# Kernel tuning notes

Hardware: AMD Instinct MI355X
Metric: run time of the kernel (lower is better)

Reference implementation:

```python
import jax, jax.numpy as jnp
import numpy as np

N_NODES = 50000
N_GRAPHS = 512


def _glorot(key, shape):
    fan_in, fan_out = shape[0], shape[1]
    lim = float(np.sqrt(6.0 / (fan_in + fan_out)))
    return jax.random.uniform(key, shape, jnp.float32, -lim, lim)


def setup_inputs() -> dict:
    key = jax.random.key(0)
    ks = jax.random.split(key, 12)
    x = jax.random.normal(ks[0], (N_NODES, 64), jnp.float32)
    edge_index = jax.random.randint(ks[1], (2, 800000), 0, N_NODES, jnp.int64)
    batch = jnp.sort(jax.random.randint(ks[2], (N_NODES,), 0, N_GRAPHS, jnp.int64))
    # GCNConv weights stored as [in, out]; bias [out]
    W1 = _glorot(ks[3], (64, 128));  b1 = jnp.zeros((128,), jnp.float32)
    W2 = _glorot(ks[4], (128, 128)); b2 = jnp.zeros((128,), jnp.float32)
    W3 = _glorot(ks[5], (128, 64));  b3 = jnp.zeros((64,), jnp.float32)
    Wl = _glorot(ks[6], (64, 10));   bl = jnp.zeros((10,), jnp.float32)
    return {"x": x, "edge_index": edge_index, "batch": batch,
            "W1": W1, "b1": b1, "W2": W2, "b2": b2,
            "W3": W3, "b3": b3, "Wl": Wl, "bl": bl}


def _gcn_conv(h_in, W, b, row, col, dinv, n):
    # GCNConv: out = D^{-1/2} (A + I) D^{-1/2} (X W) + b, self-loops folded in
    h = h_in @ W                                   # [N, out]
    norm = (dinv[row] * dinv[col])[:, None]        # [E, 1]
    agg = jax.ops.segment_sum(h[row] * norm, col, num_segments=n)
    agg = agg + (dinv * dinv)[:, None] * h          # self-loop contribution
    return agg + b


def reference(x, edge_index, batch, W1, b1, W2, b2, W3, b3, Wl, bl):
    n = x.shape[0]
    row, col = edge_index[0], edge_index[1]
    # degree of target nodes, including self loop
    deg = jax.ops.segment_sum(jnp.ones((row.shape[0],), x.dtype), col,
                              num_segments=n) + 1.0
    dinv = deg ** -0.5

    h = jax.nn.relu(_gcn_conv(x, W1, b1, row, col, dinv, n))
    h = jax.nn.relu(_gcn_conv(h, W2, b2, row, col, dinv, n))
    h = _gcn_conv(h, W3, b3, row, col, dinv, n)

    # global mean pool over graphs
    sums = jax.ops.segment_sum(h, batch, num_segments=N_GRAPHS)
    cnts = jax.ops.segment_sum(jnp.ones((n,), h.dtype), batch,
                               num_segments=N_GRAPHS)
    pooled = sums / jnp.maximum(cnts, 1.0)[:, None]
    # dropout is identity in eval mode
    return pooled @ Wl + bl
```

## Files before the change

### kernel.cpp

```cpp
#include <hip/hip_runtime.h>
#include <hip/hip_fp16.h>

typedef _Float16 f16;
typedef f16 f16x8 __attribute__((ext_vector_type(8)));
typedef float f32x4 __attribute__((ext_vector_type(4)));


__global__ void k_zero_i32(int* __restrict__ p, int n) {
    int i = blockIdx.x * blockDim.x + threadIdx.x;
    if (i < n) p[i] = 0;
}

__global__ void k_count(const int* __restrict__ col, int E, int* __restrict__ cnt) {
    int e = blockIdx.x * blockDim.x + threadIdx.x;
    if (e < E) atomicAdd(&cnt[col[e]], 1);
}

__global__ void k_bsum(const int* __restrict__ cnt, int N, int* __restrict__ bsum) {
    __shared__ int wt[4];
    int t = threadIdx.x;
    int i0 = blockIdx.x * 1024 + t * 4;
    int s = 0;
    #pragma unroll
    for (int j = 0; j < 4; ++j) { int i = i0 + j; if (i < N) s += cnt[i]; }
    #pragma unroll
    for (int off = 32; off > 0; off >>= 1) s += __shfl_down(s, off, 64);
    if ((t & 63) == 0) wt[t >> 6] = s;
    __syncthreads();
    if (t == 0) bsum[blockIdx.x] = wt[0] + wt[1] + wt[2] + wt[3];
}

__global__ void k_bscan(int* __restrict__ bsum, int nb, int* __restrict__ starts, int N) {
    int lane = threadIdx.x;
    int carry = 0;
    for (int base = 0; base < nb; base += 64) {
        int i = base + lane;
        int v = (i < nb) ? bsum[i] : 0;
        int s = v;
        #pragma unroll
        for (int off = 1; off < 64; off <<= 1) {
            int u = __shfl_up(s, off, 64);
            if (lane >= off) s += u;
        }
        if (i < nb) bsum[i] = carry + s - v;
        carry += __shfl(s, 63, 64);
    }
    if (lane == 0) starts[N] = carry;
}

__global__ void k_scan_apply(const int* __restrict__ cnt, const int* __restrict__ bsum,
                             int* __restrict__ starts, float* __restrict__ dinv, int N) {
    __shared__ int wt[4];
    int t = threadIdx.x;
    int lane = t & 63;
    int w = t >> 6;
    int i0 = blockIdx.x * 1024 + t * 4;
    int v[4];
    int ts = 0;
    #pragma unroll
    for (int j = 0; j < 4; ++j) { int i = i0 + j; v[j] = (i < N) ? cnt[i] : 0; ts += v[j]; }
    int s = ts;
    #pragma unroll
    for (int off = 1; off < 64; off <<= 1) {
        int u = __shfl_up(s, off, 64);
        if (lane >= off) s += u;
    }
    if (lane == 63) wt[w] = s;
    __syncthreads();
    int woff = 0;
    if (w > 0) woff = wt[0];
    if (w > 1) woff += wt[1];
    if (w > 2) woff += wt[2];
    int base = bsum[blockIdx.x] + woff + (s - ts);
    int run = base;
    #pragma unroll
    for (int j = 0; j < 4; ++j) {
        int i = i0 + j;
        if (i < N) {
            starts[i] = run;
            dinv[i] = rsqrtf((float)v[j] + 1.0f);
        }
        run += v[j];
    }
}

__global__ void k_fill_xcd(const int* __restrict__ row, const int* __restrict__ col, int E,
                           const int* __restrict__ starts, int* __restrict__ cnt,
                           int* __restrict__ csr, int N) {
    const int w = blockIdx.x & 7;
    const int chunk = blockIdx.x >> 3;
    const int nchunks = gridDim.x >> 3;
    const int W = (N + 7) / 8;
    const int c0 = w * W;
    const int c1 = min(N, c0 + W);
    const int stride = nchunks * blockDim.x;
    for (int e = chunk * blockDim.x + threadIdx.x; e < E; e += stride) {
        int c = col[e];
        if (c >= c0 && c < c1) {
            int pos = starts[c] + atomicSub(&cnt[c], 1) - 1;
            csr[pos] = row[e];
        }
    }
}

__global__ void k_prep(const float* __restrict__ x, __half* __restrict__ X16, long nx4,
                       const float* __restrict__ W1, const float* __restrict__ W2,
                       const float* __restrict__ W3, f16* __restrict__ Wt1,
                       f16* __restrict__ Wt2, f16* __restrict__ Wt3,
                       float* __restrict__ pooled, int npool) {
    long idx = (long)blockIdx.x * blockDim.x + threadIdx.x;
    if (idx < nx4) {
        long i = idx * 4;
        float4 v = *(const float4*)&x[i];
        __half2 h0 = __floats2half2_rn(v.x, v.y);
        __half2 h1 = __floats2half2_rn(v.z, v.w);
        uint2 q; q.x = *(unsigned int*)&h0; q.y = *(unsigned int*)&h1;
        *(uint2*)&X16[i] = q;
        return;
    }
    long j = idx - nx4;
    if (j < 32768) {
        if (j < 8192) {
            int k = (int)(j >> 7), m = (int)(j & 127);
            Wt1[m * 72 + k] = (f16)W1[j];
        } else if (j < 24576) {
            long u = j - 8192;
            int k = (int)(u >> 7), m = (int)(u & 127);
            Wt2[m * 136 + k] = (f16)W2[u];
        } else {
            long u = j - 24576;
            int k = (int)(u >> 6), m = (int)(u & 63);
            Wt3[m * 136 + k] = (f16)W3[u];
        }
        return;
    }
    long z = j - 32768;
    if (z < npool) pooled[z] = 0.0f;
}


template<int K, int M, bool BIAS, bool RELU, typename OT>
__global__ __launch_bounds__(256) void k_gemm_mfma(const f16* __restrict__ A,
                                                   const f16* __restrict__ Wt,
                                                   const float* __restrict__ bias,
                                                   OT* __restrict__ P, int N) {
    constexpr int KP = K + 8;
    constexpr int KK = K / 32;
    __shared__ f16 Wl[M * KP];
    const int t = threadIdx.x;
    constexpr int CH = (M * KP * 2) / 16;
    {
        const uint4* src = (const uint4*)Wt;
        uint4* dst = (uint4*)Wl;
        for (int i = t; i < CH; i += 256) dst[i] = src[i];
    }
    __syncthreads();
    const int lane = t & 63;
    const int wave = t >> 6;
    const int r = lane & 15;
    const int q = lane >> 4;
    const int arow = blockIdx.x * 64 + wave * 16 + r;
    f16x8 a[KK];
    #pragma unroll
    for (int kk = 0; kk < KK; ++kk) {
        if (arow < N) a[kk] = *(const f16x8*)&A[(long)arow * K + kk * 32 + q * 8];
        else { f16x8 z = {0, 0, 0, 0, 0, 0, 0, 0}; a[kk] = z; }
    }
    const int drow0 = blockIdx.x * 64 + wave * 16 + q * 4;
    #pragma unroll
    for (int ct = 0; ct < M / 16; ++ct) {
        const int col = ct * 16 + r;
        f32x4 acc = {0.f, 0.f, 0.f, 0.f};
        #pragma unroll
        for (int kk = 0; kk < KK; ++kk) {
            f16x8 b = *(const f16x8*)&Wl[col * KP + kk * 32 + q * 8];
            acc = __builtin_amdgcn_mfma_f32_16x16x32_f16(a[kk], b, acc, 0, 0, 0);
        }
        float bb = BIAS ? bias[col] : 0.f;
        #pragma unroll
        for (int g = 0; g < 4; ++g) {
            int rr = drow0 + g;
            if (rr < N) {
                float v = acc[g] + bb;
                if (RELU) v = fmaxf(v, 0.f);
                if constexpr (__is_same(OT, f16)) P[(long)rr * M + col] = (f16)v;
                else P[(long)rr * M + col] = v;
            }
        }
    }
}


template<int M, bool BIAS, bool RELU, typename OT>
__global__ void k_agg16(const __half* __restrict__ P16, const int* __restrict__ starts,
                        const int* __restrict__ csr, const float* __restrict__ dinv,
                        const float* __restrict__ b, OT* __restrict__ H, int N) {
    constexpr int TPN = M / 8;
    constexpr int NPB = 256 / TPN;
    int local = threadIdx.x / TPN;
    int fq = threadIdx.x % TPN;
    int f0 = fq * 8;
    int c = blockIdx.x * NPB + local;
    if (c >= N) return;
    int s = starts[c], e = starts[c + 1];
    float acc[8] = {};
    int i = s;
    for (; i + 3 < e; i += 4) {
        int r0 = csr[i], r1 = csr[i + 1], r2 = csr[i + 2], r3 = csr[i + 3];
        float d0 = dinv[r0], d1 = dinv[r1], d2 = dinv[r2], d3 = dinv[r3];
        uint4 u0 = *(const uint4*)&P16[(long)r0 * M + f0];
        uint4 u1 = *(const uint4*)&P16[(long)r1 * M + f0];
        uint4 u2 = *(const uint4*)&P16[(long)r2 * M + f0];
        uint4 u3 = *(const uint4*)&P16[(long)r3 * M + f0];
        const __half2* h0 = (const __half2*)&u0;
        const __half2* h1 = (const __half2*)&u1;
        const __half2* h2 = (const __half2*)&u2;
        const __half2* h3 = (const __half2*)&u3;
        #pragma unroll
        for (int j = 0; j < 4; ++j) {
            float2 v0 = __half22float2(h0[j]);
            float2 v1 = __half22float2(h1[j]);
            float2 v2 = __half22float2(h2[j]);
            float2 v3 = __half22float2(h3[j]);
            acc[2 * j]     += v0.x * d0 + v1.x * d1 + v2.x * d2 + v3.x * d3;
            acc[2 * j + 1] += v0.y * d0 + v1.y * d1 + v2.y * d2 + v3.y * d3;
        }
    }
    for (; i < e; ++i) {
        int r0 = csr[i];
        float d0 = dinv[r0];
        uint4 u0 = *(const uint4*)&P16[(long)r0 * M + f0];
        const __half2* h0 = (const __half2*)&u0;
        #pragma unroll
        for (int j = 0; j < 4; ++j) {
            float2 v0 = __half22float2(h0[j]);
            acc[2 * j]     += v0.x * d0;
            acc[2 * j + 1] += v0.y * d0;
        }
    }
    float dc = dinv[c];
    float dc2 = dc * dc;
    uint4 us = *(const uint4*)&P16[(long)c * M + f0];
    const __half2* hs = (const __half2*)&us;
    float v[8];
    #pragma unroll
    for (int j = 0; j < 4; ++j) {
        float2 fs = __half22float2(hs[j]);
        v[2 * j]     = dc * acc[2 * j]     + dc2 * fs.x;
        v[2 * j + 1] = dc * acc[2 * j + 1] + dc2 * fs.y;
    }
    if (BIAS) {
        float4 bb0 = *(const float4*)&b[f0];
        float4 bb1 = *(const float4*)&b[f0 + 4];
        v[0] += bb0.x; v[1] += bb0.y; v[2] += bb0.z; v[3] += bb0.w;
        v[4] += bb1.x; v[5] += bb1.y; v[6] += bb1.z; v[7] += bb1.w;
    }
    if (RELU) {
        #pragma unroll
        for (int j = 0; j < 8; ++j) v[j] = fmaxf(v[j], 0.f);
    }
    if constexpr (__is_same(OT, __half)) {
        __half2 h0 = __floats2half2_rn(v[0], v[1]);
        __half2 h1 = __floats2half2_rn(v[2], v[3]);
        __half2 h2 = __floats2half2_rn(v[4], v[5]);
        __half2 h3 = __floats2half2_rn(v[6], v[7]);
        uint4 qo;
        qo.x = *(unsigned int*)&h0; qo.y = *(unsigned int*)&h1;
        qo.z = *(unsigned int*)&h2; qo.w = *(unsigned int*)&h3;
        *(uint4*)&H[(long)c * M + f0] = qo;
    } else {
        *(float4*)&H[(long)c * M + f0]     = make_float4(v[0], v[1], v[2], v[3]);
        *(float4*)&H[(long)c * M + f0 + 4] = make_float4(v[4], v[5], v[6], v[7]);
    }
}


__global__ void k_gemm_naive(const float* __restrict__ X, const float* __restrict__ W,
                             float* __restrict__ P, int N, int K, int M) {
    long idx = (long)blockIdx.x * blockDim.x + threadIdx.x;
    long total = (long)N * M;
    if (idx >= total) return;
    int n = (int)(idx / M);
    int m = (int)(idx - (long)n * M);
    const float* xr = X + (long)n * K;
    float acc = 0.0f;
    for (int k = 0; k < K; ++k) acc += xr[k] * W[k * M + m];
    P[idx] = acc;
}

template<int M>
__global__ void k_aggregate4(const float* __restrict__ P, const int* __restrict__ starts,
                             const int* __restrict__ csr, const float* __restrict__ dinv,
                             const float* __restrict__ b, float* __restrict__ H,
                             int N, int do_relu) {
    constexpr int TPN = M / 4;
    constexpr int NPB = 256 / TPN;
    int local = threadIdx.x / TPN;
    int fq = threadIdx.x % TPN;
    int c = blockIdx.x * NPB + local;
    if (c >= N) return;
    int s = starts[c], e = starts[c + 1];
    float4 acc = make_float4(0.f, 0.f, 0.f, 0.f);
    for (int i = s; i < e; ++i) {
        int r = csr[i];
        float dr = dinv[r];
        float4 p = *(const float4*)&P[(long)r * M + fq * 4];
        acc.x += p.x * dr; acc.y += p.y * dr; acc.z += p.z * dr; acc.w += p.w * dr;
    }
    float dc = dinv[c];
    float dc2 = dc * dc;
    float4 ps = *(const float4*)&P[(long)c * M + fq * 4];
    float4 bb = *(const float4*)&b[fq * 4];
    float4 v;
    v.x = dc * acc.x + dc2 * ps.x + bb.x;
    v.y = dc * acc.y + dc2 * ps.y + bb.y;
    v.z = dc * acc.z + dc2 * ps.z + bb.z;
    v.w = dc * acc.w + dc2 * ps.w + bb.w;
    if (do_relu) {
        v.x = fmaxf(v.x, 0.f); v.y = fmaxf(v.y, 0.f);
        v.z = fmaxf(v.z, 0.f); v.w = fmaxf(v.w, 0.f);
    }
    *(float4*)&H[(long)c * M + fq * 4] = v;
}


__device__ __forceinline__ int lower_bound_i(const int* __restrict__ a, int n, int key) {
    int lo = 0, hi = n;
    while (lo < hi) { int mid = (lo + hi) >> 1; if (a[mid] < key) lo = mid + 1; else hi = mid; }
    return lo;
}

__global__ void k_pool_part(const float* __restrict__ H, const int* __restrict__ batch,
                            int N, float* __restrict__ pooled) {
    const int f = threadIdx.x & 63;
    const int ln = threadIdx.x >> 6;
    int n0 = blockIdx.x * 64 + ln * 16;
    int n1 = min(n0 + 16, N);
    float acc = 0.f;
    int cur = -1;
    for (int n = n0; n < n1; ++n) {
        int g = batch[n];
        if (g != cur) {
            if (cur >= 0) atomicAdd(&pooled[cur * 64 + f], acc);
            acc = 0.f;
            cur = g;
        }
        acc += H[(long)n * 64 + f];
    }
    if (cur >= 0) atomicAdd(&pooled[cur * 64 + f], acc);
}

__global__ void k_final2(const float* __restrict__ pooled, const int* __restrict__ batch,
                         int N, const float* __restrict__ Wl, const float* __restrict__ bl,
                         float* __restrict__ out, int C) {
    __shared__ float pl[64];
    int g = blockIdx.x;
    int f = threadIdx.x;
    int lo = lower_bound_i(batch, N, g);
    int hi = lower_bound_i(batch, N, g + 1);
    float inv = 1.0f / fmaxf((float)(hi - lo), 1.0f);
    pl[f] = pooled[g * 64 + f] * inv;
    __syncthreads();
    if (f < C) {
        float o = bl[f];
        #pragma unroll 8
        for (int k = 0; k < 64; ++k) o += pl[k] * Wl[k * C + f];
        out[g * C + f] = o;
    }
}

__global__ void k_pool(const float* __restrict__ H, const int* __restrict__ batch,
                       int N, int M, float* __restrict__ pooled) {
    int g = blockIdx.x;
    int f = threadIdx.x;
    int lo = lower_bound_i(batch, N, g);
    int hi = lower_bound_i(batch, N, g + 1);
    float acc = 0.0f;
    for (int n = lo; n < hi; ++n) acc += H[(long)n * M + f];
    float inv = 1.0f / fmaxf((float)(hi - lo), 1.0f);
    pooled[(long)g * M + f] = acc * inv;
}

__global__ void k_final(const float* __restrict__ pooled, const float* __restrict__ Wl,
                        const float* __restrict__ bl, float* __restrict__ out,
                        int Gn, int F, int C) {
    int idx = blockIdx.x * blockDim.x + threadIdx.x;
    if (idx >= Gn * C) return;
    int g = idx / C;
    int j = idx - g * C;
    float acc = bl[j];
    for (int f = 0; f < F; ++f) acc += pooled[g * F + f] * Wl[f * C + j];
    out[idx] = acc;
}


extern "C" void kernel_launch(void* const* d_in, const int* in_sizes, int n_in,
                              void* d_out, int out_size, void* d_ws, size_t ws_size,
                              hipStream_t stream) {
    const float* x  = (const float*)d_in[0];
    const int*   ei = (const int*)d_in[1];
    const int*   batch = (const int*)d_in[2];
    const float* W1 = (const float*)d_in[3];
    const float* b1 = (const float*)d_in[4];
    const float* W2 = (const float*)d_in[5];
    const float* b2 = (const float*)d_in[6];
    const float* W3 = (const float*)d_in[7];
    const float* b3 = (const float*)d_in[8];
    const float* Wl = (const float*)d_in[9];
    const float* bl = (const float*)d_in[10];

    const int N  = in_sizes[2];
    const int E  = in_sizes[1] / 2;
    const int C  = in_sizes[10];
    const int Gn = out_size / C;
    const int F1 = in_sizes[4];
    const int F2 = in_sizes[6];
    const int F3 = in_sizes[8];
    const int K0 = in_sizes[0] / N;

    const int* row = ei;
    const int* col = ei + E;

    char* base = (char*)d_ws;
    size_t off = 0;
    auto alloc = [&](size_t bytes) {
        off = (off + 63) & ~(size_t)63;
        void* p = base + off;
        off += bytes;
        return p;
    };
    int* cnt     = (int*)alloc((size_t)N * 4);
    int* starts  = (int*)alloc((size_t)(N + 1) * 4);
    int* bsum    = (int*)alloc(256 * 4);
    int* csr     = (int*)alloc((size_t)E * 4);
    float* dinv  = (float*)alloc((size_t)N * 4);
    __half* X16  = (__half*)alloc((size_t)N * 64 * 2);
    __half* AX16 = (__half*)alloc((size_t)N * 64 * 2);
    __half* H1   = (__half*)alloc((size_t)N * 128 * 2);
    __half* P16a = (__half*)alloc((size_t)N * 128 * 2);
    __half* B16  = (__half*)alloc((size_t)N * 128 * 2);
    __half* P16b = (__half*)alloc((size_t)N * 64 * 2);
    float* H3    = (float*)alloc((size_t)N * 64 * 4);
    f16* Wt1     = (f16*)alloc((size_t)128 * 72 * 2);
    f16* Wt2     = (f16*)alloc((size_t)128 * 136 * 2);
    f16* Wt3     = (f16*)alloc((size_t)64 * 136 * 2);
    float* pooled = (float*)alloc((size_t)Gn * 64 * 4);
    float* Afb   = (float*)alloc((size_t)N * 128 * 4);
    float* Bfb   = (float*)alloc((size_t)N * 128 * 4);

    const int BLK = 256;
    auto blocks = [](long n, int b) { return (int)((n + b - 1) / b); };
    const int nb = blocks(N, 1024);

    k_zero_i32<<<blocks(N, BLK), BLK, 0, stream>>>(cnt, N);
    k_count<<<blocks(E, BLK), BLK, 0, stream>>>(col, E, cnt);
    k_bsum<<<nb, 256, 0, stream>>>(cnt, N, bsum);
    k_bscan<<<1, 64, 0, stream>>>(bsum, nb, starts, N);
    k_scan_apply<<<nb, 256, 0, stream>>>(cnt, bsum, starts, dinv, N);
    k_fill_xcd<<<128 * 8, 256, 0, stream>>>(row, col, E, starts, cnt, csr, N);

    const bool fast = (K0 == 64 && F1 == 128 && F2 == 128 && F3 == 64);

    if (fast) {
        long nx4 = (long)N * 64 / 4;
        long prep_threads = nx4 + 32768 + (long)Gn * 64;
        k_prep<<<blocks(prep_threads, BLK), BLK, 0, stream>>>(
            x, X16, nx4, W1, W2, W3, Wt1, Wt2, Wt3, pooled, Gn * 64);

        k_agg16<64, false, false, __half><<<blocks(N, 32), 256, 0, stream>>>(X16, starts, csr, dinv, nullptr, AX16, N);
        k_gemm_mfma<64, 128, true, true, f16><<<blocks(N, 64), 256, 0, stream>>>((const f16*)AX16, Wt1, b1, (f16*)H1, N);
        k_gemm_mfma<128, 128, false, false, f16><<<blocks(N, 64), 256, 0, stream>>>((const f16*)H1, Wt2, nullptr, (f16*)P16a, N);
        k_agg16<128, true, true, __half><<<blocks(N, 16), 256, 0, stream>>>(P16a, starts, csr, dinv, b2, B16, N);
        k_gemm_mfma<128, 64, false, false, f16><<<blocks(N, 64), 256, 0, stream>>>((const f16*)B16, Wt3, nullptr, (f16*)P16b, N);
        k_agg16<64, true, false, float><<<blocks(N, 32), 256, 0, stream>>>(P16b, starts, csr, dinv, b3, H3, N);
        k_pool_part<<<blocks(N, 64), 256, 0, stream>>>(H3, batch, N, pooled);
        k_final2<<<Gn, 64, 0, stream>>>(pooled, batch, N, Wl, bl, (float*)d_out, C);
    } else {
        k_gemm_naive<<<blocks((long)N * F1, BLK), BLK, 0, stream>>>(x, W1, Afb, N, K0, F1);
        k_aggregate4<128><<<blocks(N, 8), 256, 0, stream>>>(Afb, starts, csr, dinv, b1, Bfb, N, 1);
        k_gemm_naive<<<blocks((long)N * F2, BLK), BLK, 0, stream>>>(Bfb, W2, Afb, N, F1, F2);
        k_aggregate4<128><<<blocks(N, 8), 256, 0, stream>>>(Afb, starts, csr, dinv, b2, Bfb, N, 1);
        k_gemm_naive<<<blocks((long)N * F3, BLK), BLK, 0, stream>>>(Bfb, W3, Afb, N, F2, F3);
        k_aggregate4<64><<<blocks(N, 16), 256, 0, stream>>>(Afb, starts, csr, dinv, b3, Bfb, N, 0);
        k_pool<<<Gn, F3, 0, stream>>>(Bfb, batch, N, F3, pooled);
        k_final<<<blocks(Gn * C, BLK), BLK, 0, stream>>>(pooled, Wl, bl, (float*)d_out, Gn, F3, C);
    }
}
```

Baseline: 204.8 us.

## Sort nodes by in-degree to balance aggregation wavefronts

Adds a degree histogram, scan and scatter that build a permutation of nodes grouped by in-degree, and the three aggregation kernels now process nodes in that order. The aim is to cut divergence inside a wavefront, where neighbouring nodes with very different edge counts keep lanes idle. It also folds the count-array zeroing into the prep kernel to save a launch. The cost is three extra small kernels and an indirection through perm, plus writes to the output in scattered order, which loses locality.

```diff
diff --git a/kernel.cpp b/kernel.cpp
--- a/kernel.cpp
+++ b/kernel.cpp
@@ -103,11 +103,47 @@
     }
 }
 
+__global__ void k_dhist(const int* __restrict__ starts, int N, int* __restrict__ hist) {
+    __shared__ int lh[64];
+    if (threadIdx.x < 64) lh[threadIdx.x] = 0;
+    __syncthreads();
+    int i = blockIdx.x * blockDim.x + threadIdx.x;
+    if (i < N) {
+        int d = starts[i + 1] - starts[i];
+        atomicAdd(&lh[min(d, 63)], 1);
+    }
+    __syncthreads();
+    if (threadIdx.x < 64 && lh[threadIdx.x]) atomicAdd(&hist[threadIdx.x], lh[threadIdx.x]);
+}
+
+__global__ void k_dscan(int* __restrict__ hist) {
+    int lane = threadIdx.x;
+    int v = hist[lane];
+    int s = v;
+    #pragma unroll
+    for (int off = 1; off < 64; off <<= 1) {
+        int u = __shfl_up(s, off, 64);
+        if (lane >= off) s += u;
+    }
+    hist[lane] = s - v;
+}
+
+__global__ void k_dscatter(const int* __restrict__ starts, int N,
+                           int* __restrict__ binoff, int* __restrict__ perm) {
+    int i = blockIdx.x * blockDim.x + threadIdx.x;
+    if (i < N) {
+        int d = starts[i + 1] - starts[i];
+        int pos = atomicAdd(&binoff[min(d, 63)], 1);
+        perm[pos] = i;
+    }
+}
+
 __global__ void k_prep(const float* __restrict__ x, __half* __restrict__ X16, long nx4,
                        const float* __restrict__ W1, const float* __restrict__ W2,
                        const float* __restrict__ W3, f16* __restrict__ Wt1,
                        f16* __restrict__ Wt2, f16* __restrict__ Wt3,
-                       float* __restrict__ pooled, int npool) {
+                       float* __restrict__ pooled, int npool,
+                       int* __restrict__ cnt, int N, int* __restrict__ hist) {
     long idx = (long)blockIdx.x * blockDim.x + threadIdx.x;
     if (idx < nx4) {
         long i = idx * 4;
@@ -135,7 +171,11 @@
         return;
     }
     long z = j - 32768;
-    if (z < npool) pooled[z] = 0.0f;
+    if (z < npool) { pooled[z] = 0.0f; return; }
+    long y = z - npool;
+    if (y < N) { cnt[y] = 0; return; }
+    long h = y - N;
+    if (h < 64) hist[h] = 0;
 }
 
 
@@ -194,14 +234,16 @@
 template<int M, bool BIAS, bool RELU, typename OT>
 __global__ void k_agg16(const __half* __restrict__ P16, const int* __restrict__ starts,
                         const int* __restrict__ csr, const float* __restrict__ dinv,
-                        const float* __restrict__ b, OT* __restrict__ H, int N) {
+                        const float* __restrict__ b, OT* __restrict__ H, int N,
+                        const int* __restrict__ perm) {
     constexpr int TPN = M / 8;
     constexpr int NPB = 256 / TPN;
     int local = threadIdx.x / TPN;
     int fq = threadIdx.x % TPN;
     int f0 = fq * 8;
-    int c = blockIdx.x * NPB + local;
-    if (c >= N) return;
+    int gi = blockIdx.x * NPB + local;
+    if (gi >= N) return;
+    int c = perm[gi];
     int s = starts[c], e = starts[c + 1];
     float acc[8] = {};
     int i = s;
@@ -434,6 +476,8 @@
     int* bsum    = (int*)alloc(256 * 4);
     int* csr     = (int*)alloc((size_t)E * 4);
     float* dinv  = (float*)alloc((size_t)N * 4);
+    int* hist    = (int*)alloc(64 * 4);
+    int* perm    = (int*)alloc((size_t)N * 4);
     __half* X16  = (__half*)alloc((size_t)N * 64 * 2);
     __half* AX16 = (__half*)alloc((size_t)N * 64 * 2);
     __half* H1   = (__half*)alloc((size_t)N * 128 * 2);
@@ -452,27 +496,34 @@
     auto blocks = [](long n, int b) { return (int)((n + b - 1) / b); };
     const int nb = blocks(N, 1024);
 
-    k_zero_i32<<<blocks(N, BLK), BLK, 0, stream>>>(cnt, N);
+    const bool fast = (K0 == 64 && F1 == 128 && F2 == 128 && F3 == 64);
+
+    if (fast) {
+        long nx4 = (long)N * 64 / 4;
+        long prep_threads = nx4 + 32768 + (long)Gn * 64 + N + 64;
+        k_prep<<<blocks(prep_threads, BLK), BLK, 0, stream>>>(
+            x, X16, nx4, W1, W2, W3, Wt1, Wt2, Wt3, pooled, Gn * 64, cnt, N, hist);
+    } else {
+        k_zero_i32<<<blocks(N, BLK), BLK, 0, stream>>>(cnt, N);
+    }
+
     k_count<<<blocks(E, BLK), BLK, 0, stream>>>(col, E, cnt);
     k_bsum<<<nb, 256, 0, stream>>>(cnt, N, bsum);
     k_bscan<<<1, 64, 0, stream>>>(bsum, nb, starts, N);
     k_scan_apply<<<nb, 256, 0, stream>>>(cnt, bsum, starts, dinv, N);
     k_fill_xcd<<<128 * 8, 256, 0, stream>>>(row, col, E, starts, cnt, csr, N);
 
-    const bool fast = (K0 == 64 && F1 == 128 && F2 == 128 && F3 == 64);
-
     if (fast) {
-        long nx4 = (long)N * 64 / 4;
-        long prep_threads = nx4 + 32768 + (long)Gn * 64;
-        k_prep<<<blocks(prep_threads, BLK), BLK, 0, stream>>>(
-            x, X16, nx4, W1, W2, W3, Wt1, Wt2, Wt3, pooled, Gn * 64);
-
-        k_agg16<64, false, false, __half><<<blocks(N, 32), 256, 0, stream>>>(X16, starts, csr, dinv, nullptr, AX16, N);
+        k_dhist<<<blocks(N, BLK), BLK, 0, stream>>>(starts, N, hist);
+        k_dscan<<<1, 64, 0, stream>>>(hist);
+        k_dscatter<<<blocks(N, BLK), BLK, 0, stream>>>(starts, N, hist, perm);
+
+        k_agg16<64, false, false, __half><<<blocks(N, 32), 256, 0, stream>>>(X16, starts, csr, dinv, nullptr, AX16, N, perm);
         k_gemm_mfma<64, 128, true, true, f16><<<blocks(N, 64), 256, 0, stream>>>((const f16*)AX16, Wt1, b1, (f16*)H1, N);
         k_gemm_mfma<128, 128, false, false, f16><<<blocks(N, 64), 256, 0, stream>>>((const f16*)H1, Wt2, nullptr, (f16*)P16a, N);
-        k_agg16<128, true, true, __half><<<blocks(N, 16), 256, 0, stream>>>(P16a, starts, csr, dinv, b2, B16, N);
+        k_agg16<128, true, true, __half><<<blocks(N, 16), 256, 0, stream>>>(P16a, starts, csr, dinv, b2, B16, N, perm);
         k_gemm_mfma<128, 64, false, false, f16><<<blocks(N, 64), 256, 0, stream>>>((const f16*)B16, Wt3, nullptr, (f16*)P16b, N);
-        k_agg16<64, true, false, float><<<blocks(N, 32), 256, 0, stream>>>(P16b, starts, csr, dinv, b3, H3, N);
+        k_agg16<64, true, false, float><<<blocks(N, 32), 256, 0, stream>>>(P16b, starts, csr, dinv, b3, H3, N, perm);
         k_pool_part<<<blocks(N, 64), 256, 0, stream>>>(H3, batch, N, pooled);
         k_final2<<<Gn, 64, 0, stream>>>(pooled, batch, N, Wl, bl, (float*)d_out, C);
     } else {
```

Measured after the change: 365.5 us. 78.5% more time.
